# Optimization experiments

Measured on AMD Instinct MI355X. Metric: run time of the kernel, lower is better.

## Reference

```python
import jax, jax.numpy as jnp
import numpy as np

N = 50000
NEG_SLOPE = 0.2  # PyG GATConv default leaky_relu slope


def _gat_layer(x, src, dst, W, a_s, a_d, b):
    # x: [N, Fin]; W: [Fin, H*C]; a_s, a_d: [H, C]; b: [C]
    H, C = a_s.shape
    xp = (x @ W).reshape(N, H, C)                      # projected node features per head
    alpha_s = jnp.einsum('nhc,hc->nh', xp, a_s)        # [N, H]
    alpha_d = jnp.einsum('nhc,hc->nh', xp, a_d)        # [N, H]
    e = jax.nn.leaky_relu(alpha_s[src] + alpha_d[dst], NEG_SLOPE)  # [E, H]
    # segment softmax over incoming edges of each dst node
    m = jax.ops.segment_max(e, dst, num_segments=N)
    m = jnp.where(jnp.isfinite(m), m, 0.0)
    p = jnp.exp(e - jax.lax.stop_gradient(m)[dst])
    denom = jax.ops.segment_sum(p, dst, num_segments=N)
    alpha = p / denom[dst]                             # [E, H]
    # scatter-aggregate messages
    out = jax.ops.segment_sum(alpha[:, :, None] * xp[src], dst, num_segments=N)  # [N, H, C]
    return out.mean(axis=1) + b                        # concat=False -> mean over heads


def setup_inputs() -> dict:
    key = jax.random.key(0)
    ks = jax.random.split(key, 16)
    IN, HID, OUT, H = 128, 64, 40, 4
    E = 800000
    x = jax.random.normal(ks[0], (N, IN), dtype=jnp.float32)
    edge_index = jax.random.randint(ks[1], (2, E), 0, N, dtype=jnp.int64)

    def mk(kw, ka, fin, fout):
        s = 1.0 / np.sqrt(fin)
        W = jax.random.normal(kw, (fin, H * fout), dtype=jnp.float32) * s
        a_s = jax.random.normal(ka, (H, fout), dtype=jnp.float32) * 0.1
        a_d = jax.random.normal(jax.random.fold_in(ka, 1), (H, fout), dtype=jnp.float32) * 0.1
        b = jnp.zeros((fout,), dtype=jnp.float32)
        return W, a_s, a_d, b

    W1, as1, ad1, b1 = mk(ks[2], ks[3], IN, HID)
    W2, as2, ad2, b2 = mk(ks[4], ks[5], HID, HID)
    W3, as3, ad3, b3 = mk(ks[6], ks[7], HID, OUT)
    return dict(x=x, edge_index=edge_index,
                W1=W1, as1=as1, ad1=ad1, b1=b1,
                W2=W2, as2=as2, ad2=ad2, b2=b2,
                W3=W3, as3=as3, ad3=ad3, b3=b3)


def reference(x, edge_index, W1, as1, ad1, b1, W2, as2, ad2, b2, W3, as3, ad3, b3):
    # PyG GATConv adds self-loops by default
    loop = jnp.arange(N, dtype=edge_index.dtype)
    src = jnp.concatenate([edge_index[0], loop])
    dst = jnp.concatenate([edge_index[1], loop])
    h = jax.nn.relu(_gat_layer(x, src, dst, W1, as1, ad1, b1))   # dropout is identity in eval
    h = jax.nn.relu(_gat_layer(h, src, dst, W2, as2, ad2, b2))
    h = jax.nn.relu(_gat_layer(h, src, dst, W3, as3, ad3, b3))
    return jax.nn.log_softmax(h, axis=-1)
```

## Files before the change

### kernel.cpp

```cpp
#include <hip/hip_runtime.h>
#include <math.h>

#define NNODES 50000
#define NEG_SLOPE 0.2f

typedef unsigned short ushort8v __attribute__((ext_vector_type(8)));
typedef unsigned short ushort4v __attribute__((ext_vector_type(4)));
typedef short short8v __attribute__((ext_vector_type(8)));
typedef float f32x4 __attribute__((ext_vector_type(4)));
typedef float f32x2 __attribute__((ext_vector_type(2)));

__device__ __forceinline__ float bf2f(unsigned short u){ return __uint_as_float(((unsigned)u) << 16); }
__device__ __forceinline__ unsigned short f2bf(float f){
    unsigned u = __float_as_uint(f);
    u += 0x7fff + ((u >> 16) & 1);
    return (unsigned short)(u >> 16);
}

__global__ void detect_kernel(const unsigned long long* __restrict__ e, int* __restrict__ flag){
    const unsigned long long v = e[threadIdx.x & 63];
    const unsigned long long mask = __ballot(v >= (1ULL << 32));
    if(threadIdx.x == 0) *flag = (mask == 0ULL) ? 1 : 0;
}

__global__ void convert_kernel(const void* __restrict__ e, const int* __restrict__ flag,
                               int* __restrict__ out, int* __restrict__ deg,
                               int total, int E){
    int i = blockIdx.x * blockDim.x + threadIdx.x;
    if(i < total){
        int v;
        if(*flag) v = (int)((const long long*)e)[i];
        else      v = ((const int*)e)[i];
        out[i] = v;
        if(i >= E) atomicAdd(&deg[v], 1);
    }
}

__global__ void f2bf_kernel(const float* __restrict__ in, unsigned short* __restrict__ out, int total4){
    const int i = blockIdx.x * blockDim.x + threadIdx.x;
    if(i < total4){
        const float4 v = *(const float4*)&in[(size_t)i * 4];
        ushort4v o;
        o[0] = f2bf(v.x); o[1] = f2bf(v.y); o[2] = f2bf(v.z); o[3] = f2bf(v.w);
        *(ushort4v*)&out[(size_t)i * 4] = o;
    }
}

__device__ __forceinline__ void emit_wt(const float* __restrict__ W, const float* __restrict__ a_s,
                                        const float* __restrict__ a_d, unsigned short* __restrict__ Wt,
                                        int K, int NC, int C, int id){
    const int n = id / K, k = id - n * K;
    float v;
    if(n < NC){
        v = W[(size_t)k * NC + n];
    } else {
        const int h = n - NC;
        const int hh = h & 3;
        const float* av = (h < 4) ? a_s : a_d;
        v = 0.f;
        for(int c = 0; c < C; c++) v += W[(size_t)k * NC + hh * C + c] * av[hh * C + c];
    }
    Wt[(size_t)n * K + k] = f2bf(v);
}

__global__ void prep_kernel(const float* __restrict__ W1, const float* __restrict__ as1, const float* __restrict__ ad1,
                            const float* __restrict__ W2, const float* __restrict__ as2, const float* __restrict__ ad2,
                            const float* __restrict__ W3, const float* __restrict__ as3, const float* __restrict__ ad3,
                            unsigned short* __restrict__ W1t, unsigned short* __restrict__ W2t,
                            unsigned short* __restrict__ W3t){
    int id = blockIdx.x * blockDim.x + threadIdx.x;
    if(id < 264 * 128){ emit_wt(W1, as1, ad1, W1t, 128, 256, 64, id); return; }
    id -= 264 * 128;
    if(id < 264 * 64){ emit_wt(W2, as2, ad2, W2t, 64, 256, 64, id); return; }
    id -= 264 * 64;
    if(id < 168 * 64){ emit_wt(W3, as3, ad3, W3t, 64, 160, 40, id); }
}

__global__ __launch_bounds__(512) void scan1_kernel(const int* __restrict__ deg,
                                                    int* __restrict__ excl,
                                                    int* __restrict__ bsum, int n){
    __shared__ int sh[512];
    const int t = threadIdx.x;
    const int gid = blockIdx.x * 512 + t;
    const int v = (gid < n) ? deg[gid] : 0;
    sh[t] = v;
    __syncthreads();
    for(int off = 1; off < 512; off <<= 1){
        const int add = (t >= off) ? sh[t - off] : 0;
        __syncthreads();
        sh[t] += add;
        __syncthreads();
    }
    if(gid < n) excl[gid] = sh[t] - v;
    if(t == 511) bsum[blockIdx.x] = sh[511];
}

__global__ __launch_bounds__(128) void scan2_kernel(int* __restrict__ bsum, int nb){
    __shared__ int sh[128];
    const int t = threadIdx.x;
    const int v = (t < nb) ? bsum[t] : 0;
    sh[t] = v;
    __syncthreads();
    for(int off = 1; off < 128; off <<= 1){
        const int add = (t >= off) ? sh[t - off] : 0;
        __syncthreads();
        sh[t] += add;
        __syncthreads();
    }
    if(t < nb) bsum[t] = sh[t] - v;
}

__global__ void scan3_kernel(const int* __restrict__ excl, const int* __restrict__ bsum,
                             int* __restrict__ row_ptr, int* __restrict__ cursor,
                             int n, int E){
    const int gid = blockIdx.x * blockDim.x + threadIdx.x;
    if(gid < n){
        const int r = excl[gid] + bsum[gid >> 9];
        row_ptr[gid] = r;
        cursor[gid] = r;
    }
    if(gid == 0) row_ptr[n] = E;
}

__global__ void scatter_kernel(const int* __restrict__ src, const int* __restrict__ dst,
                               int* __restrict__ cursor, int* __restrict__ col, int E){
    int i = blockIdx.x * blockDim.x + threadIdx.x;
    if(i < E){
        int d = dst[i];
        int pos = atomicAdd(&cursor[d], 1);
        col[pos] = src[i];
    }
}

template<int K, int NC>
__global__ __launch_bounds__(256) void mfma_gemm_kernel(const unsigned short* __restrict__ A,
                                                        const unsigned short* __restrict__ Bt,
                                                        unsigned short* __restrict__ C,
                                                        f32x2* __restrict__ ea,
                                                        f32x2* __restrict__ ed,
                                                        int M){
    constexpr int NT = NC / 16 + 1;
    const int lane = threadIdx.x & 63;
    const int wave = threadIdx.x >> 6;
    const int quad = lane >> 4;
    const int l16 = lane & 15;
    const int bm = blockIdx.x * 64;
    const int m = min(bm + wave * 16 + l16, M - 1);
    const size_t arow = (size_t)m * K;

    f32x4 acc[NT];
    #pragma unroll
    for(int t = 0; t < NT; t++) acc[t] = (f32x4){0,0,0,0};
    int cn[NT];
    #pragma unroll
    for(int t = 0; t < NT; t++) cn[t] = min(t * 16 + l16, NC + 7);

    for(int k0 = 0; k0 < K; k0 += 32){
        const short8v a = *(const short8v*)&A[arow + k0 + quad * 8];
        #pragma unroll
        for(int t = 0; t < NT; t++){
            const short8v b = *(const short8v*)&Bt[(size_t)cn[t] * K + k0 + quad * 8];
            acc[t] = __builtin_amdgcn_mfma_f32_16x16x32_bf16(a, b, acc[t], 0, 0, 0);
        }
    }
    const int rbase = bm + wave * 16 + quad * 4;
    #pragma unroll
    for(int t = 0; t < NT - 1; t++){
        const int c = t * 16 + l16;
        #pragma unroll
        for(int r = 0; r < 4; r++){
            const int row = rbase + r;
            if(row < M) C[(size_t)row * NC + c] = f2bf(acc[t][r]);
        }
    }
    if(l16 < 8){
        const int h = l16 & 3;
        f32x2* dst = (l16 < 4) ? ea : ed;
        #pragma unroll
        for(int r = 0; r < 4; r++){
            const int row = rbase + r;
            if(row < M){
                const float v = acc[NT - 1][r];
                f32x2 e2 = {__expf(v), __expf(NEG_SLOPE * v)};
                dst[(size_t)row * 4 + h] = e2;
            }
        }
    }
}

template<int C, bool FINAL>
__global__ __launch_bounds__(256) void gather_kernel(const unsigned short* __restrict__ xp,
                                                     const int* __restrict__ row_ptr,
                                                     const int* __restrict__ col,
                                                     const f32x2* __restrict__ ea,
                                                     const f32x2* __restrict__ ed,
                                                     const float* __restrict__ bias,
                                                     void* __restrict__ outv){
    constexpr int HC = 4 * C;
    constexpr int LPE = HC / 8;
    __shared__ float sbuf[4][FINAL ? HC : 1];
    const int lane = threadIdx.x & 63;
    const int wave = threadIdx.x >> 6;
    const int n = blockIdx.x * 4 + wave;
    const int half = lane >> 5;
    const int hl = lane & 31;
    const bool active = hl < LPE;
    const int head = min((8 * hl) / C, 3);
    const int rs = row_ptr[n], re = row_ptr[n + 1];
    const int T = re - rs + 1;
    const f32x2 edh = ed[(size_t)n * 4 + head];
    const unsigned short* xpl = xp + 8 * hl;

    f32x2 acc2[4] = {{0,0},{0,0},{0,0},{0,0}};
    float denom = 0.f;
    int k = 0;
    for(; k + 4 <= T; k += 4){
        const int eA = rs + k + half;
        const int eB = eA + 2;
        const int sA = (eA < re) ? col[eA] : n;
        const int sB = (eB < re) ? col[eB] : n;
        const f32x2 a2 = ea[(size_t)sA * 4 + head];
        const f32x2 b2 = ea[(size_t)sB * 4 + head];
        const float wA = fmaxf(a2[0] * edh[0], a2[1] * edh[1]);
        const float wB = fmaxf(b2[0] * edh[0], b2[1] * edh[1]);
        denom += wA + wB;
        if(active){
            const uint4 uA = *(const uint4*)&xpl[(size_t)sA * HC];
            const uint4 uB = *(const uint4*)&xpl[(size_t)sB * HC];
            const f32x2 wA2 = {wA, wA};
            const f32x2 wB2 = {wB, wB};
            acc2[0] += wA2 * (f32x2){__uint_as_float(uA.x << 16), __uint_as_float(uA.x & 0xffff0000u)};
            acc2[1] += wA2 * (f32x2){__uint_as_float(uA.y << 16), __uint_as_float(uA.y & 0xffff0000u)};
            acc2[2] += wA2 * (f32x2){__uint_as_float(uA.z << 16), __uint_as_float(uA.z & 0xffff0000u)};
            acc2[3] += wA2 * (f32x2){__uint_as_float(uA.w << 16), __uint_as_float(uA.w & 0xffff0000u)};
            acc2[0] += wB2 * (f32x2){__uint_as_float(uB.x << 16), __uint_as_float(uB.x & 0xffff0000u)};
            acc2[1] += wB2 * (f32x2){__uint_as_float(uB.y << 16), __uint_as_float(uB.y & 0xffff0000u)};
            acc2[2] += wB2 * (f32x2){__uint_as_float(uB.z << 16), __uint_as_float(uB.z & 0xffff0000u)};
            acc2[3] += wB2 * (f32x2){__uint_as_float(uB.w << 16), __uint_as_float(uB.w & 0xffff0000u)};
        }
    }
    for(; k + 2 <= T; k += 2){
        const int e = rs + k + half;
        const int s = (e < re) ? col[e] : n;
        const f32x2 a2 = ea[(size_t)s * 4 + head];
        const float wh = fmaxf(a2[0] * edh[0], a2[1] * edh[1]);
        denom += wh;
        if(active){
            const uint4 u = *(const uint4*)&xpl[(size_t)s * HC];
            const f32x2 w2 = {wh, wh};
            acc2[0] += w2 * (f32x2){__uint_as_float(u.x << 16), __uint_as_float(u.x & 0xffff0000u)};
            acc2[1] += w2 * (f32x2){__uint_as_float(u.y << 16), __uint_as_float(u.y & 0xffff0000u)};
            acc2[2] += w2 * (f32x2){__uint_as_float(u.z << 16), __uint_as_float(u.z & 0xffff0000u)};
            acc2[3] += w2 * (f32x2){__uint_as_float(u.w << 16), __uint_as_float(u.w & 0xffff0000u)};
        }
    }
    if(k < T && half == 0){
        const int e = rs + k;
        const int s = (e < re) ? col[e] : n;
        const f32x2 a2 = ea[(size_t)s * 4 + head];
        const float wh = fmaxf(a2[0] * edh[0], a2[1] * edh[1]);
        denom += wh;
        if(active){
            const uint4 u = *(const uint4*)&xpl[(size_t)s * HC];
            const f32x2 w2 = {wh, wh};
            acc2[0] += w2 * (f32x2){__uint_as_float(u.x << 16), __uint_as_float(u.x & 0xffff0000u)};
            acc2[1] += w2 * (f32x2){__uint_as_float(u.y << 16), __uint_as_float(u.y & 0xffff0000u)};
            acc2[2] += w2 * (f32x2){__uint_as_float(u.z << 16), __uint_as_float(u.z & 0xffff0000u)};
            acc2[3] += w2 * (f32x2){__uint_as_float(u.w << 16), __uint_as_float(u.w & 0xffff0000u)};
        }
    }
    #pragma unroll
    for(int p = 0; p < 4; p++){
        acc2[p][0] += __shfl_xor(acc2[p][0], 32);
        acc2[p][1] += __shfl_xor(acc2[p][1], 32);
    }
    denom += __shfl_xor(denom, 32);
    const float ih = 1.f / denom;
    float acc[8];
    #pragma unroll
    for(int p = 0; p < 4; p++){ acc[2*p] = acc2[p][0] * ih; acc[2*p+1] = acc2[p][1] * ih; }

    if(!FINAL){
        #pragma unroll
        for(int j = 0; j < 8; j++){
            acc[j] += __shfl_xor(acc[j], 8);
            acc[j] += __shfl_xor(acc[j], 16);
        }
        if(lane < 8){
            unsigned short* out = (unsigned short*)outv;
            ushort8v o;
            #pragma unroll
            for(int j = 0; j < 8; j++)
                o[j] = f2bf(fmaxf(acc[j] * 0.25f + bias[8 * lane + j], 0.f));
            *(ushort8v*)&out[(size_t)n * C + 8 * lane] = o;
        }
    } else {
        if(active && half == 0){
            #pragma unroll
            for(int j = 0; j < 8; j++) sbuf[wave][8 * hl + j] = acc[j];
        }
        __syncthreads();
        float* out = (float*)outv;
        float4 o = {0,0,0,0};
        if(lane < 10){
            const int c = 4 * lane;
            #pragma unroll
            for(int h = 0; h < 4; h++){
                o.x += sbuf[wave][h * 40 + c + 0];
                o.y += sbuf[wave][h * 40 + c + 1];
                o.z += sbuf[wave][h * 40 + c + 2];
                o.w += sbuf[wave][h * 40 + c + 3];
            }
            const float4 b4 = *(const float4*)&bias[c];
            o.x = fmaxf(o.x * 0.25f + b4.x, 0.f);
            o.y = fmaxf(o.y * 0.25f + b4.y, 0.f);
            o.z = fmaxf(o.z * 0.25f + b4.z, 0.f);
            o.w = fmaxf(o.w * 0.25f + b4.w, 0.f);
        }
        float lm = (lane < 10) ? fmaxf(fmaxf(o.x, o.y), fmaxf(o.z, o.w)) : -INFINITY;
        #pragma unroll
        for(int off = 8; off; off >>= 1) lm = fmaxf(lm, __shfl_xor(lm, off));
        float se = 0.f;
        if(lane < 10) se = __expf(o.x-lm) + __expf(o.y-lm) + __expf(o.z-lm) + __expf(o.w-lm);
        #pragma unroll
        for(int off = 8; off; off >>= 1) se += __shfl_xor(se, off);
        const float logZ = lm + logf(se);
        if(lane < 10){
            float4 r = {o.x - logZ, o.y - logZ, o.z - logZ, o.w - logZ};
            *(float4*)&out[(size_t)n * 40 + 4 * lane] = r;
        }
    }
}

extern "C" void kernel_launch(void* const* d_in, const int* in_sizes, int n_in,
                              void* d_out, int out_size, void* d_ws, size_t ws_size,
                              hipStream_t stream){
    const int N = NNODES;
    const int E = in_sizes[1] / 2;

    const float* x   = (const float*)d_in[0];
    const float* W1  = (const float*)d_in[2];
    const float* as1 = (const float*)d_in[3];
    const float* ad1 = (const float*)d_in[4];
    const float* b1  = (const float*)d_in[5];
    const float* W2  = (const float*)d_in[6];
    const float* as2 = (const float*)d_in[7];
    const float* ad2 = (const float*)d_in[8];
    const float* b2  = (const float*)d_in[9];
    const float* W3  = (const float*)d_in[10];
    const float* as3 = (const float*)d_in[11];
    const float* ad3 = (const float*)d_in[12];
    const float* b3  = (const float*)d_in[13];

    char* ws = (char*)d_ws;
    size_t off = 0;
    auto alloc = [&](size_t bytes) -> void* {
        void* p = ws + off;
        off = (off + bytes + 255) & ~(size_t)255;
        return p;
    };
    int*   flag    = (int*)  alloc(4);
    int*   e32     = (int*)  alloc((size_t)2 * E * 4);
    int*   row_ptr = (int*)  alloc((size_t)(N + 1) * 4);
    int*   colv    = (int*)  alloc((size_t)E * 4);
    int*   cursor  = (int*)  alloc((size_t)N * 4);
    int*   deg     = (int*)  alloc((size_t)N * 4);
    int*   excl    = (int*)  alloc((size_t)N * 4);
    int*   bsum    = (int*)  alloc(128 * 4);
    unsigned short* xp  = (unsigned short*)alloc((size_t)N * 256 * 2);
    unsigned short* xbf = (unsigned short*)alloc((size_t)N * 128 * 2);
    unsigned short* W1t = (unsigned short*)alloc((size_t)264 * 128 * 2);
    unsigned short* W2t = (unsigned short*)alloc((size_t)264 * 64 * 2);
    unsigned short* W3t = (unsigned short*)alloc((size_t)168 * 64 * 2);
    f32x2* eav     = (f32x2*)alloc((size_t)N * 4 * 8);
    f32x2* edv     = (f32x2*)alloc((size_t)N * 4 * 8);
    unsigned short* h = (unsigned short*)alloc((size_t)N * 64 * 2);
    (void)ws_size;

    hipMemsetAsync(deg, 0, (size_t)N * 4, stream);
    detect_kernel<<<1, 64, 0, stream>>>((const unsigned long long*)d_in[1], flag);
    convert_kernel<<<(2 * E + 255) / 256, 256, 0, stream>>>(d_in[1], flag, e32, deg, 2 * E, E);
    const int* srcv = e32;
    const int* dstv = e32 + E;

    f2bf_kernel<<<(N * 128 / 4 + 255) / 256, 256, 0, stream>>>(x, xbf, N * 128 / 4);
    const int prepTotal = 264 * 128 + 264 * 64 + 168 * 64;
    prep_kernel<<<(prepTotal + 255) / 256, 256, 0, stream>>>(W1, as1, ad1, W2, as2, ad2,
                                                             W3, as3, ad3, W1t, W2t, W3t);

    const int nbScan = (N + 511) / 512;
    scan1_kernel<<<nbScan, 512, 0, stream>>>(deg, excl, bsum, N);
    scan2_kernel<<<1, 128, 0, stream>>>(bsum, nbScan);
    scan3_kernel<<<(N + 255) / 256, 256, 0, stream>>>(excl, bsum, row_ptr, cursor, N, E);
    scatter_kernel<<<(E + 255) / 256, 256, 0, stream>>>(srcv, dstv, cursor, colv, E);

    const int nodeBlocks = N / 4;
    const int mBlocks = (N + 63) / 64;

    mfma_gemm_kernel<128, 256><<<mBlocks, 256, 0, stream>>>(xbf, W1t, xp, eav, edv, N);
    gather_kernel<64, false><<<nodeBlocks, 256, 0, stream>>>(xp, row_ptr, colv, eav, edv, b1, h);

    mfma_gemm_kernel<64, 256><<<mBlocks, 256, 0, stream>>>(h, W2t, xp, eav, edv, N);
    gather_kernel<64, false><<<nodeBlocks, 256, 0, stream>>>(xp, row_ptr, colv, eav, edv, b2, h);

    mfma_gemm_kernel<64, 160><<<mBlocks, 256, 0, stream>>>(h, W3t, xp, eav, edv, N);
    gather_kernel<40, true><<<nodeBlocks, 256, 0, stream>>>(xp, row_ptr, colv, eav, edv, b3, (float*)d_out);
}
```

Measured before the change: 483.2 us.

## Drop edge int32 conversion, fuse prep kernels, split GEMM columns, unroll gather

Removes the separate edge conversion pass. The degree histogram and scatter now read the raw int64/int32 edge index directly, and the memset and dtype detection are merged into one init kernel. The x-to-bf16 conversion is folded into the weight prep kernel. The MFMA GEMM is split across a second grid dimension over 64-column tiles, with only the first tile computing attention logits, to raise parallelism and cut per-block register pressure. The gather main loop is unrolled from 2 to 4 edges per half-wave so more loads are in flight, at the cost of extra registers and re-reading A per column tile.

```diff
diff --git a/kernel.cpp b/kernel.cpp
--- a/kernel.cpp
+++ b/kernel.cpp
@@ -17,63 +17,24 @@
     return (unsigned short)(u >> 16);
 }
 
-__global__ void detect_kernel(const unsigned long long* __restrict__ e, int* __restrict__ flag){
-    const unsigned long long v = e[threadIdx.x & 63];
-    const unsigned long long mask = __ballot(v >= (1ULL << 32));
-    if(threadIdx.x == 0) *flag = (mask == 0ULL) ? 1 : 0;
-}
-
-__global__ void convert_kernel(const void* __restrict__ e, const int* __restrict__ flag,
-                               int* __restrict__ out, int* __restrict__ deg,
-                               int total, int E){
-    int i = blockIdx.x * blockDim.x + threadIdx.x;
-    if(i < total){
-        int v;
-        if(*flag) v = (int)((const long long*)e)[i];
-        else      v = ((const int*)e)[i];
-        out[i] = v;
-        if(i >= E) atomicAdd(&deg[v], 1);
-    }
-}
-
-__global__ void f2bf_kernel(const float* __restrict__ in, unsigned short* __restrict__ out, int total4){
+__global__ void init_kernel(const unsigned long long* __restrict__ e, int* __restrict__ flag,
+                            int* __restrict__ deg, int N){
+    if(blockIdx.x == 0 && threadIdx.x < 64){
+        const unsigned long long v = e[threadIdx.x];
+        const unsigned long long mask = __ballot(v >= (1ULL << 32));
+        if(threadIdx.x == 0) *flag = (mask == 0ULL) ? 1 : 0;
+    }
+    for(int i = blockIdx.x * blockDim.x + threadIdx.x; i < N; i += gridDim.x * blockDim.x)
+        deg[i] = 0;
+}
+
+__global__ void hist_kernel(const void* __restrict__ e, const int* __restrict__ flag,
+                            int* __restrict__ deg, int E){
     const int i = blockIdx.x * blockDim.x + threadIdx.x;
-    if(i < total4){
-        const float4 v = *(const float4*)&in[(size_t)i * 4];
-        ushort4v o;
-        o[0] = f2bf(v.x); o[1] = f2bf(v.y); o[2] = f2bf(v.z); o[3] = f2bf(v.w);
-        *(ushort4v*)&out[(size_t)i * 4] = o;
-    }
-}
-
-__device__ __forceinline__ void emit_wt(const float* __restrict__ W, const float* __restrict__ a_s,
-                                        const float* __restrict__ a_d, unsigned short* __restrict__ Wt,
-                                        int K, int NC, int C, int id){
-    const int n = id / K, k = id - n * K;
-    float v;
-    if(n < NC){
-        v = W[(size_t)k * NC + n];
-    } else {
-        const int h = n - NC;
-        const int hh = h & 3;
-        const float* av = (h < 4) ? a_s : a_d;
-        v = 0.f;
-        for(int c = 0; c < C; c++) v += W[(size_t)k * NC + hh * C + c] * av[hh * C + c];
-    }
-    Wt[(size_t)n * K + k] = f2bf(v);
-}
-
-__global__ void prep_kernel(const float* __restrict__ W1, const float* __restrict__ as1, const float* __restrict__ ad1,
-                            const float* __restrict__ W2, const float* __restrict__ as2, const float* __restrict__ ad2,
-                            const float* __restrict__ W3, const float* __restrict__ as3, const float* __restrict__ ad3,
-                            unsigned short* __restrict__ W1t, unsigned short* __restrict__ W2t,
-                            unsigned short* __restrict__ W3t){
-    int id = blockIdx.x * blockDim.x + threadIdx.x;
-    if(id < 264 * 128){ emit_wt(W1, as1, ad1, W1t, 128, 256, 64, id); return; }
-    id -= 264 * 128;
-    if(id < 264 * 64){ emit_wt(W2, as2, ad2, W2t, 64, 256, 64, id); return; }
-    id -= 264 * 64;
-    if(id < 168 * 64){ emit_wt(W3, as3, ad3, W3t, 64, 160, 40, id); }
+    if(i < E){
+        const int d = (*flag) ? (int)((const long long*)e)[E + i] : ((const int*)e)[E + i];
+        atomicAdd(&deg[d], 1);
+    }
 }
 
 __global__ __launch_bounds__(512) void scan1_kernel(const int* __restrict__ deg,
@@ -122,14 +83,55 @@
     if(gid == 0) row_ptr[n] = E;
 }
 
-__global__ void scatter_kernel(const int* __restrict__ src, const int* __restrict__ dst,
+__global__ void scatter_kernel(const void* __restrict__ e, const int* __restrict__ flag,
                                int* __restrict__ cursor, int* __restrict__ col, int E){
-    int i = blockIdx.x * blockDim.x + threadIdx.x;
+    const int i = blockIdx.x * blockDim.x + threadIdx.x;
     if(i < E){
-        int d = dst[i];
-        int pos = atomicAdd(&cursor[d], 1);
-        col[pos] = src[i];
-    }
+        int s, d;
+        if(*flag){ s = (int)((const long long*)e)[i]; d = (int)((const long long*)e)[E + i]; }
+        else     { s = ((const int*)e)[i];            d = ((const int*)e)[E + i]; }
+        const int pos = atomicAdd(&cursor[d], 1);
+        col[pos] = s;
+    }
+}
+
+__device__ __forceinline__ void emit_wt(const float* __restrict__ W, const float* __restrict__ a_s,
+                                        const float* __restrict__ a_d, unsigned short* __restrict__ Wt,
+                                        int K, int NC, int C, int id){
+    const int n = id / K, k = id - n * K;
+    float v;
+    if(n < NC){
+        v = W[(size_t)k * NC + n];
+    } else {
+        const int h = n - NC;
+        const int hh = h & 3;
+        const float* av = (h < 4) ? a_s : a_d;
+        v = 0.f;
+        for(int c = 0; c < C; c++) v += W[(size_t)k * NC + hh * C + c] * av[hh * C + c];
+    }
+    Wt[(size_t)n * K + k] = f2bf(v);
+}
+
+__global__ void prep_kernel(const float* __restrict__ x, unsigned short* __restrict__ xbf, int X4,
+                            const float* __restrict__ W1, const float* __restrict__ as1, const float* __restrict__ ad1,
+                            const float* __restrict__ W2, const float* __restrict__ as2, const float* __restrict__ ad2,
+                            const float* __restrict__ W3, const float* __restrict__ as3, const float* __restrict__ ad3,
+                            unsigned short* __restrict__ W1t, unsigned short* __restrict__ W2t,
+                            unsigned short* __restrict__ W3t){
+    int id = blockIdx.x * blockDim.x + threadIdx.x;
+    if(id < X4){
+        const float4 v = *(const float4*)&x[(size_t)id * 4];
+        ushort4v o;
+        o[0] = f2bf(v.x); o[1] = f2bf(v.y); o[2] = f2bf(v.z); o[3] = f2bf(v.w);
+        *(ushort4v*)&xbf[(size_t)id * 4] = o;
+        return;
+    }
+    id -= X4;
+    if(id < 264 * 128){ emit_wt(W1, as1, ad1, W1t, 128, 256, 64, id); return; }
+    id -= 264 * 128;
+    if(id < 264 * 64){ emit_wt(W2, as2, ad2, W2t, 64, 256, 64, id); return; }
+    id -= 264 * 64;
+    if(id < 168 * 64){ emit_wt(W3, as3, ad3, W3t, 64, 160, 40, id); }
 }
 
 template<int K, int NC>
@@ -139,48 +141,54 @@
                                                         f32x2* __restrict__ ea,
                                                         f32x2* __restrict__ ed,
                                                         int M){
-    constexpr int NT = NC / 16 + 1;
     const int lane = threadIdx.x & 63;
     const int wave = threadIdx.x >> 6;
     const int quad = lane >> 4;
     const int l16 = lane & 15;
     const int bm = blockIdx.x * 64;
+    const int bn = blockIdx.y * 64;
+    const int nt = (blockIdx.y == 0) ? 5 : 4;
     const int m = min(bm + wave * 16 + l16, M - 1);
     const size_t arow = (size_t)m * K;
 
-    f32x4 acc[NT];
+    f32x4 acc[5];
     #pragma unroll
-    for(int t = 0; t < NT; t++) acc[t] = (f32x4){0,0,0,0};
-    int cn[NT];
+    for(int t = 0; t < 5; t++) acc[t] = (f32x4){0,0,0,0};
+    int cn[5];
     #pragma unroll
-    for(int t = 0; t < NT; t++) cn[t] = min(t * 16 + l16, NC + 7);
+    for(int t = 0; t < 4; t++) cn[t] = min(bn + t * 16 + l16, NC - 1);
+    cn[4] = NC + min(l16, 7);
 
     for(int k0 = 0; k0 < K; k0 += 32){
         const short8v a = *(const short8v*)&A[arow + k0 + quad * 8];
         #pragma unroll
-        for(int t = 0; t < NT; t++){
-            const short8v b = *(const short8v*)&Bt[(size_t)cn[t] * K + k0 + quad * 8];
-            acc[t] = __builtin_amdgcn_mfma_f32_16x16x32_bf16(a, b, acc[t], 0, 0, 0);
+        for(int t = 0; t < 5; t++){
+            if(t < nt){
+                const short8v b = *(const short8v*)&Bt[(size_t)cn[t] * K + k0 + quad * 8];
+                acc[t] = __builtin_amdgcn_mfma_f32_16x16x32_bf16(a, b, acc[t], 0, 0, 0);
+            }
         }
     }
     const int rbase = bm + wave * 16 + quad * 4;
     #pragma unroll
-    for(int t = 0; t < NT - 1; t++){
-        const int c = t * 16 + l16;
-        #pragma unroll
-        for(int r = 0; r < 4; r++){
-            const int row = rbase + r;
-            if(row < M) C[(size_t)row * NC + c] = f2bf(acc[t][r]);
-        }
-    }
-    if(l16 < 8){
+    for(int t = 0; t < 4; t++){
+        const int c = bn + t * 16 + l16;
+        if(c < NC){
+            #pragma unroll
+            for(int r = 0; r < 4; r++){
+                const int row = rbase + r;
+                if(row < M) C[(size_t)row * NC + c] = f2bf(acc[t][r]);
+            }
+        }
+    }
+    if(blockIdx.y == 0 && l16 < 8){
         const int h = l16 & 3;
         f32x2* dst = (l16 < 4) ? ea : ed;
         #pragma unroll
         for(int r = 0; r < 4; r++){
             const int row = rbase + r;
             if(row < M){
-                const float v = acc[NT - 1][r];
+                const float v = acc[4][r];
                 f32x2 e2 = {__expf(v), __expf(NEG_SLOPE * v)};
                 dst[(size_t)row * 4 + h] = e2;
             }
@@ -214,29 +222,43 @@
     f32x2 acc2[4] = {{0,0},{0,0},{0,0},{0,0}};
     float denom = 0.f;
     int k = 0;
-    for(; k + 4 <= T; k += 4){
-        const int eA = rs + k + half;
-        const int eB = eA + 2;
-        const int sA = (eA < re) ? col[eA] : n;
-        const int sB = (eB < re) ? col[eB] : n;
-        const f32x2 a2 = ea[(size_t)sA * 4 + head];
-        const f32x2 b2 = ea[(size_t)sB * 4 + head];
-        const float wA = fmaxf(a2[0] * edh[0], a2[1] * edh[1]);
-        const float wB = fmaxf(b2[0] * edh[0], b2[1] * edh[1]);
-        denom += wA + wB;
+    for(; k + 8 <= T; k += 8){
+        const int e0 = rs + k + half, e1 = e0 + 2, e2 = e0 + 4, e3 = e0 + 6;
+        const int s0 = (e0 < re) ? col[e0] : n;
+        const int s1 = (e1 < re) ? col[e1] : n;
+        const int s2 = (e2 < re) ? col[e2] : n;
+        const int s3 = (e3 < re) ? col[e3] : n;
+        const f32x2 a0 = ea[(size_t)s0 * 4 + head];
+        const f32x2 a1 = ea[(size_t)s1 * 4 + head];
+        const f32x2 a2 = ea[(size_t)s2 * 4 + head];
+        const f32x2 a3 = ea[(size_t)s3 * 4 + head];
+        const float w0 = fmaxf(a0[0] * edh[0], a0[1] * edh[1]);
+        const float w1 = fmaxf(a1[0] * edh[0], a1[1] * edh[1]);
+        const float w2 = fmaxf(a2[0] * edh[0], a2[1] * edh[1]);
+        const float w3 = fmaxf(a3[0] * edh[0], a3[1] * edh[1]);
+        denom += (w0 + w1) + (w2 + w3);
         if(active){
-            const uint4 uA = *(const uint4*)&xpl[(size_t)sA * HC];
-            const uint4 uB = *(const uint4*)&xpl[(size_t)sB * HC];
-            const f32x2 wA2 = {wA, wA};
-            const f32x2 wB2 = {wB, wB};
-            acc2[0] += wA2 * (f32x2){__uint_as_float(uA.x << 16), __uint_as_float(uA.x & 0xffff0000u)};
-            acc2[1] += wA2 * (f32x2){__uint_as_float(uA.y << 16), __uint_as_float(uA.y & 0xffff0000u)};
-            acc2[2] += wA2 * (f32x2){__uint_as_float(uA.z << 16), __uint_as_float(uA.z & 0xffff0000u)};
-            acc2[3] += wA2 * (f32x2){__uint_as_float(uA.w << 16), __uint_as_float(uA.w & 0xffff0000u)};
-            acc2[0] += wB2 * (f32x2){__uint_as_float(uB.x << 16), __uint_as_float(uB.x & 0xffff0000u)};
-            acc2[1] += wB2 * (f32x2){__uint_as_float(uB.y << 16), __uint_as_float(uB.y & 0xffff0000u)};
-            acc2[2] += wB2 * (f32x2){__uint_as_float(uB.z << 16), __uint_as_float(uB.z & 0xffff0000u)};
-            acc2[3] += wB2 * (f32x2){__uint_as_float(uB.w << 16), __uint_as_float(uB.w & 0xffff0000u)};
+            const uint4 u0 = *(const uint4*)&xpl[(size_t)s0 * HC];
+            const uint4 u1 = *(const uint4*)&xpl[(size_t)s1 * HC];
+            const uint4 u2 = *(const uint4*)&xpl[(size_t)s2 * HC];
+            const uint4 u3 = *(const uint4*)&xpl[(size_t)s3 * HC];
+            const f32x2 W0 = {w0, w0}, W1 = {w1, w1}, W2 = {w2, w2}, W3 = {w3, w3};
+            acc2[0] += W0 * (f32x2){__uint_as_float(u0.x << 16), __uint_as_float(u0.x & 0xffff0000u)};
+            acc2[1] += W0 * (f32x2){__uint_as_float(u0.y << 16), __uint_as_float(u0.y & 0xffff0000u)};
+            acc2[2] += W0 * (f32x2){__uint_as_float(u0.z << 16), __uint_as_float(u0.z & 0xffff0000u)};
+            acc2[3] += W0 * (f32x2){__uint_as_float(u0.w << 16), __uint_as_float(u0.w & 0xffff0000u)};
+            acc2[0] += W1 * (f32x2){__uint_as_float(u1.x << 16), __uint_as_float(u1.x & 0xffff0000u)};
+            acc2[1] += W1 * (f32x2){__uint_as_float(u1.y << 16), __uint_as_float(u1.y & 0xffff0000u)};
+            acc2[2] += W1 * (f32x2){__uint_as_float(u1.z << 16), __uint_as_float(u1.z & 0xffff0000u)};
+            acc2[3] += W1 * (f32x2){__uint_as_float(u1.w << 16), __uint_as_float(u1.w & 0xffff0000u)};
+            acc2[0] += W2 * (f32x2){__uint_as_float(u2.x << 16), __uint_as_float(u2.x & 0xffff0000u)};
+            acc2[1] += W2 * (f32x2){__uint_as_float(u2.y << 16), __uint_as_float(u2.y & 0xffff0000u)};
+            acc2[2] += W2 * (f32x2){__uint_as_float(u2.z << 16), __uint_as_float(u2.z & 0xffff0000u)};
+            acc2[3] += W2 * (f32x2){__uint_as_float(u2.w << 16), __uint_as_float(u2.w & 0xffff0000u)};
+            acc2[0] += W3 * (f32x2){__uint_as_float(u3.x << 16), __uint_as_float(u3.x & 0xffff0000u)};
+            acc2[1] += W3 * (f32x2){__uint_as_float(u3.y << 16), __uint_as_float(u3.y & 0xffff0000u)};
+            acc2[2] += W3 * (f32x2){__uint_as_float(u3.z << 16), __uint_as_float(u3.z & 0xffff0000u)};
+            acc2[3] += W3 * (f32x2){__uint_as_float(u3.w << 16), __uint_as_float(u3.w & 0xffff0000u)};
         }
     }
     for(; k + 2 <= T; k += 2){
@@ -360,7 +382,6 @@
         return p;
     };
     int*   flag    = (int*)  alloc(4);
-    int*   e32     = (int*)  alloc((size_t)2 * E * 4);
     int*   row_ptr = (int*)  alloc((size_t)(N + 1) * 4);
     int*   colv    = (int*)  alloc((size_t)E * 4);
     int*   cursor  = (int*)  alloc((size_t)N * 4);
@@ -377,32 +398,32 @@
     unsigned short* h = (unsigned short*)alloc((size_t)N * 64 * 2);
     (void)ws_size;
 
-    hipMemsetAsync(deg, 0, (size_t)N * 4, stream);
-    detect_kernel<<<1, 64, 0, stream>>>((const unsigned long long*)d_in[1], flag);
-    convert_kernel<<<(2 * E + 255) / 256, 256, 0, stream>>>(d_in[1], flag, e32, deg, 2 * E, E);
-    const int* srcv = e32;
-    const int* dstv = e32 + E;
-
-    f2bf_kernel<<<(N * 128 / 4 + 255) / 256, 256, 0, stream>>>(x, xbf, N * 128 / 4);
-    const int prepTotal = 264 * 128 + 264 * 64 + 168 * 64;
-    prep_kernel<<<(prepTotal + 255) / 256, 256, 0, stream>>>(W1, as1, ad1, W2, as2, ad2,
+    const void* eraw = d_in[1];
+
+    init_kernel<<<(N + 255) / 256, 256, 0, stream>>>((const unsigned long long*)eraw, flag, deg, N);
+    hist_kernel<<<(E + 255) / 256, 256, 0, stream>>>(eraw, flag, deg, E);
+
+    const int X4 = N * 128 / 4;
+    const int prepTotal = X4 + 264 * 128 + 264 * 64 + 168 * 64;
+    prep_kernel<<<(prepTotal + 255) / 256, 256, 0, stream>>>(x, xbf, X4,
+                                                             W1, as1, ad1, W2, as2, ad2,
                                                              W3, as3, ad3, W1t, W2t, W3t);
 
     const int nbScan = (N + 511) / 512;
     scan1_kernel<<<nbScan, 512, 0, stream>>>(deg, excl, bsum, N);
     scan2_kernel<<<1, 128, 0, stream>>>(bsum, nbScan);
     scan3_kernel<<<(N + 255) / 256, 256, 0, stream>>>(excl, bsum, row_ptr, cursor, N, E);
-    scatter_kernel<<<(E + 255) / 256, 256, 0, stream>>>(srcv, dstv, cursor, colv, E);
+    scatter_kernel<<<(E + 255) / 256, 256, 0, stream>>>(eraw, flag, cursor, colv, E);
 
     const int nodeBlocks = N / 4;
     const int mBlocks = (N + 63) / 64;
 
-    mfma_gemm_kernel<128, 256><<<mBlocks, 256, 0, stream>>>(xbf, W1t, xp, eav, edv, N);
+    mfma_gemm_kernel<128, 256><<<dim3(mBlocks, 4), 256, 0, stream>>>(xbf, W1t, xp, eav, edv, N);
     gather_kernel<64, false><<<nodeBlocks, 256, 0, stream>>>(xp, row_ptr, colv, eav, edv, b1, h);
 
-    mfma_gemm_kernel<64, 256><<<mBlocks, 256, 0, stream>>>(h, W2t, xp, eav, edv, N);
+    mfma_gemm_kernel<64, 256><<<dim3(mBlocks, 4), 256, 0, stream>>>(h, W2t, xp, eav, edv, N);
     gather_kernel<64, false><<<nodeBlocks, 256, 0, stream>>>(xp, row_ptr, colv, eav, edv, b2, h);
 
-    mfma_gemm_kernel<64, 160><<<mBlocks, 256, 0, stream>>>(h, W3t, xp, eav, edv, N);
+    mfma_gemm_kernel<64, 160><<<dim3(mBlocks, 3), 256, 0, stream>>>(h, W3t, xp, eav, edv, N);
     gather_kernel<40, true><<<nodeBlocks, 256, 0, stream>>>(xp, row_ptr, colv, eav, edv, b3, (float*)d_out);
 }
```

New measurement: 462.9 us. -4.2%, faster.
